# Kernel tuning notes

Hardware: AMD Instinct MI355X
Metric: run time of the kernel (lower is better)

## Reference

```python
import jax, jax.numpy as jnp
import numpy as np

NUM_USER = 100000
NUM_ITEM = 50000
DIM = 64
NUM_EDGES = 3200000


def setup_inputs() -> dict:
    key = jax.random.key(0)
    k1, k2, k3, k4 = jax.random.split(key, 4)
    return {
        "user_embedding": jax.random.normal(k1, (NUM_USER, DIM), dtype=jnp.float32),
        "item_embedding": jax.random.normal(k2, (NUM_ITEM, DIM), dtype=jnp.float32),
        "edge_user": jax.random.randint(k3, (NUM_EDGES,), 0, NUM_USER, dtype=jnp.int32).astype(jnp.int64),
        "edge_item": jax.random.randint(k4, (NUM_EDGES,), 0, NUM_ITEM, dtype=jnp.int32).astype(jnp.int64),
    }


def _segment_mean(feats, idx, num_segments):
    # scatter_mean semantics: sum per segment / count, empty segments -> 0
    s = jax.ops.segment_sum(feats, idx, num_segments=num_segments)  # [n, dim]
    cnt = jax.ops.segment_sum(jnp.ones((idx.shape[0], 1), feats.dtype), idx,
                              num_segments=num_segments)  # [n, 1]
    return s / jnp.maximum(cnt, 1.0)


def reference(user_embedding, item_embedding, edge_user, edge_item):
    num_user = user_embedding.shape[0]
    num_item = item_embedding.shape[0]

    # view1: aggregate_neighbor_features — mean of purchased-item embeddings per user
    neighbor_feat = _segment_mean(item_embedding[edge_item], edge_user, num_user)

    # view2: aggregate_cooccurrence_features — two-stage mean aggregation
    # stage 1: per item, mean of its purchasers' embeddings
    item_user_agg = _segment_mean(user_embedding[edge_user], edge_item, num_item)
    # stage 2: per user, mean of stage-1 features of purchased items
    cooccur_feat = _segment_mean(item_user_agg[edge_item], edge_user, num_user)

    return (neighbor_feat, cooccur_feat)
```

## Files before the change

### kernel.cpp

```cpp
#include <hip/hip_runtime.h>
#include <hip/hip_fp16.h>

constexpr int NUM_USER  = 100000;
constexpr int NUM_ITEM  = 50000;
constexpr int DIM       = 64;
constexpr int NUM_EDGES = 3200000;

constexpr int KPB   = 64;
constexpr int NB_U  = (NUM_USER + KPB - 1) / KPB;
constexpr int NB_I  = (NUM_ITEM + KPB - 1) / KPB;
constexpr int HKEY  = 32;
constexpr int CHUNK = 4096;
constexpr int CSH   = 14;
constexpr int NCH_I = 4;
constexpr int NCH_U = 7;
constexpr int CAP_U = 2560;
constexpr int CAP_I = 4608;

__device__ __forceinline__ __half2 u2h(unsigned u) {
  union { unsigned u; __half2 h; } v; v.u = u; return v.h;
}
__device__ __forceinline__ unsigned h2u(__half2 h) {
  union { __half2 h; unsigned u; } v; v.h = h; return v.u;
}

__device__ __forceinline__ int detect64(const void* eu, const void* ei) {
  const int* a = (const int*)eu;
  const int* b = (const int*)ei;
  int any = 0;
#pragma unroll
  for (int i = 1; i < 64; i += 2) { any |= a[i]; any |= b[i]; }
  return any == 0;
}

__device__ __forceinline__ int idx_at(const void* p, int e, int is64) {
  return is64 ? ((const int*)p)[2 * e] : ((const int*)p)[e];
}

__global__ void k_cvt(const float* __restrict__ ue, unsigned* __restrict__ u32,
                      const float* __restrict__ ie, unsigned* __restrict__ fused) {
  const int nu = NUM_USER * 32, ni = NUM_ITEM * 32;
  for (int t = blockIdx.x * blockDim.x + threadIdx.x; t < nu + ni;
       t += gridDim.x * blockDim.x) {
    if (t < nu) {
      const float2 v = ((const float2*)ue)[t];
      u32[t] = h2u(__floats2half2_rn(v.x, v.y));
    } else {
      const int s = t - nu;
      const float2 v = ((const float2*)ie)[s];
      fused[(size_t)(s >> 5) * 64 + 2 * (s & 31)] = h2u(__floats2half2_rn(v.x, v.y));
    }
  }
}

__global__ void k_part2(const void* eu_p, const void* ei_p,
                        int* gcur_i, unsigned int* __restrict__ pairs_i,
                        int* gcur_u, unsigned int* __restrict__ pairs_u,
                        int capI, int capU) {
  __shared__ int hist_u[NB_U], base_u[NB_U];
  __shared__ int hist_i[NB_I], base_i[NB_I];
  for (int t = threadIdx.x; t < NB_U; t += blockDim.x) hist_u[t] = 0;
  for (int t = threadIdx.x; t < NB_I; t += blockDim.x) hist_i[t] = 0;
  __syncthreads();
  const int is64 = detect64(eu_p, ei_p);
  const int ch = NUM_EDGES / gridDim.x;
  const int lo = blockIdx.x * ch, hiE = lo + ch;
  for (int e = lo + threadIdx.x; e < hiE; e += blockDim.x) {
    atomicAdd(&hist_u[idx_at(eu_p, e, is64) >> 6], 1);
    atomicAdd(&hist_i[idx_at(ei_p, e, is64) >> 6], 1);
  }
  __syncthreads();
  for (int t = threadIdx.x; t < NB_U; t += blockDim.x) {
    const int h = hist_u[t];
    int b = 0;
    if (h) {
      b = atomicAdd(&gcur_u[t], h);
      if (capU) b += t * capU;
    }
    base_u[t] = b;
    hist_u[t] = 0;
  }
  for (int t = threadIdx.x; t < NB_I; t += blockDim.x) {
    const int h = hist_i[t];
    int b = 0;
    if (h) {
      b = atomicAdd(&gcur_i[t], h);
      if (capI) b += t * capI;
    }
    base_i[t] = b;
    hist_i[t] = 0;
  }
  __syncthreads();
  for (int e = lo + threadIdx.x; e < hiE; e += blockDim.x) {
    const int eu = idx_at(eu_p, e, is64);
    const int ei = idx_at(ei_p, e, is64);
    const int bi = ei >> 6;
    const int pi = base_i[bi] + atomicAdd(&hist_i[bi], 1);
    if (!capI || pi < (bi + 1) * capI)
      pairs_i[pi] = ((unsigned)(ei & 63) << 17) | (unsigned)eu;
    const int bu = eu >> 6;
    const int pu = base_u[bu] + atomicAdd(&hist_u[bu], 1);
    if (!capU || pu < (bu + 1) * capU)
      pairs_u[pu] = ((unsigned)(eu & 63) << 17) | (unsigned)ei;
  }
}

__global__ void k_hist_part(const void* eu_p, const void* ei_p,
                            int* __restrict__ partials) {
  __shared__ int hu[NB_U];
  __shared__ int hi_[NB_I];
  for (int t = threadIdx.x; t < NB_U; t += blockDim.x) hu[t] = 0;
  for (int t = threadIdx.x; t < NB_I; t += blockDim.x) hi_[t] = 0;
  __syncthreads();
  const int is64 = detect64(eu_p, ei_p);
  const int ga = gridDim.x;
  const int ch = NUM_EDGES / ga;
  const int b = blockIdx.x;
  const int lo = b * ch, hiE = lo + ch;
  for (int e = lo + threadIdx.x; e < hiE; e += blockDim.x) {
    atomicAdd(&hu[idx_at(eu_p, e, is64) >> 6], 1);
    atomicAdd(&hi_[idx_at(ei_p, e, is64) >> 6], 1);
  }
  __syncthreads();
  int* pu = partials;
  int* pi = partials + (size_t)NB_U * ga;
  for (int t = threadIdx.x; t < NB_U; t += blockDim.x) pu[(size_t)t * ga + b] = hu[t];
  for (int t = threadIdx.x; t < NB_I; t += blockDim.x) pi[(size_t)t * ga + b] = hi_[t];
}

__global__ void k_hist_reduce(const int* __restrict__ partials, int ga,
                              int* __restrict__ gcnt_u, int* __restrict__ gcnt_i) {
  const int k = blockIdx.x * blockDim.x + threadIdx.x;
  if (k >= NB_U + NB_I) return;
  const int* base = (k < NB_U) ? partials + (size_t)k * ga
                               : partials + (size_t)NB_U * ga + (size_t)(k - NB_U) * ga;
  int s = 0;
  for (int b = 0; b < ga; ++b) s += base[b];
  if (k < NB_U) gcnt_u[k] = s;
  else          gcnt_i[k - NB_U] = s;
}

__device__ void scan_body(const int* __restrict__ in, int* __restrict__ out,
                          int* __restrict__ cur, int n) {
  __shared__ int part[1024];
  const int t = threadIdx.x;
  const int chunk = (n + 1023) >> 10;
  const int lo = min(t * chunk, n);
  const int hi = min(lo + chunk, n);
  int s = 0;
  for (int i = lo; i < hi; ++i) s += in[i];
  part[t] = s;
  __syncthreads();
  for (int d = 1; d < 1024; d <<= 1) {
    int v = (t >= d) ? part[t - d] : 0;
    __syncthreads();
    part[t] += v;
    __syncthreads();
  }
  int run = (t == 0) ? 0 : part[t - 1];
  for (int i = lo; i < hi; ++i) {
    int v = in[i];
    out[i] = run; cur[i] = run; run += v;
  }
  if (t == 1023) out[n] = part[1023];
}

__global__ void k_scan2(const int* cu, int* bu, int* curu,
                        const int* ci, int* bi, int* curi) {
  if (blockIdx.x == 0) scan_body(cu, bu, curu, NB_U);
  else                 scan_body(ci, bi, curi, NB_I);
}

__device__ __forceinline__ void decode_bucket(int g, int NB, int& bucket, int& half) {
  const int G = (NB * 2) >> 4;
  if (g < G * 16) {
    const int q = g >> 4, r = g & 15;
    bucket = q * 8 + (r & 7);
    half = r >> 3;
  } else {
    const int idx = g - G * 16;
    bucket = G * 8 + (idx >> 1);
    half = idx & 1;
  }
}

__device__ __forceinline__ void bucket_extent(int bucket, const int* gbase,
                                              const int* gcnt, int cap,
                                              int& lo, int& hi) {
  if (cap > 0) {
    lo = bucket * cap;
    hi = lo + min(gcnt[bucket], cap);
  } else {
    lo = gbase[bucket];
    hi = gbase[bucket + 1];
  }
}

__global__ __launch_bounds__(256, 8)
void k_agg_item(const unsigned* __restrict__ user32,
                const unsigned int* __restrict__ pairs,
                const int* __restrict__ gbase, const int* __restrict__ gcnt,
                int cap, unsigned* __restrict__ fused) {
  constexpr int NBINS = NCH_U * HKEY;
  __shared__ int sorted[CHUNK];
  __shared__ int hist[NBINS], base[NBINS], cur[NBINS];
  __shared__ int gsum[NCH_U];
  const int tid = threadIdx.x;
  const int lane = tid & 63;
  const int wid = tid >> 6;
  const int half = lane >> 5;
  const int c = lane & 31;
  int bucket, key_half;
  decode_bucket(blockIdx.x, NB_I, bucket, key_half);
  const int key0 = key_half * HKEY;
  int lo, hi;
  bucket_extent(bucket, gbase, gcnt, cap, lo, hi);

  unsigned s[8]; int cnt[8];
#pragma unroll
  for (int r = 0; r < 8; ++r) { s[r] = 0u; cnt[r] = 0; }

  for (int clo = lo; clo < hi; clo += CHUNK) {
    const int csz = min(CHUNK, hi - clo);
    for (int t = tid; t < NBINS; t += 256) hist[t] = 0;
    __syncthreads();
    for (int j = tid; j < csz; j += 256) {
      const unsigned p = pairs[clo + j];
      const int k = (int)(p >> 17) - key0;
      if ((unsigned)k < HKEY) {
        const int ch = (int)(p & 0x1FFFF) >> CSH;
        atomicAdd(&hist[ch * HKEY + k], 1);
      }
    }
    __syncthreads();
    if (tid < NCH_U) {
      int g = 0;
      for (int q = 0; q < HKEY; ++q) g += hist[tid * HKEY + q];
      gsum[tid] = g;
    }
    __syncthreads();
    for (int t = tid; t < NBINS; t += 256) {
      const int ch = t >> 5;
      int b = 0;
      for (int q = 0; q < ch; ++q) b += gsum[q];
      for (int q = ch * HKEY; q < t; ++q) b += hist[q];
      base[t] = b; cur[t] = b;
    }
    __syncthreads();
    for (int j = tid; j < csz; j += 256) {
      const unsigned p = pairs[clo + j];
      const int k = (int)(p >> 17) - key0;
      if ((unsigned)k < HKEY) {
        const int v = (int)(p & 0x1FFFF);
        const int slot = atomicAdd(&cur[(v >> CSH) * HKEY + k], 1);
        sorted[slot] = v;
      }
    }
    __syncthreads();
    for (int ch = 0; ch < NCH_U; ++ch) {
#pragma unroll
      for (int r = 0; r < 8; ++r) {
        const int bin = ch * HKEY + wid * 8 + r;
        const int jlo = base[bin], jhi = cur[bin];
        cnt[r] += jhi - jlo;
        for (int j = jlo; j < jhi; j += 8) {
          unsigned w[4];
#pragma unroll
          for (int q = 0; q < 4; ++q) {
            const int jj = j + 2 * q + half;
            w[q] = (jj < jhi) ? user32[(size_t)sorted[jj] * 32 + c] : 0u;
          }
#pragma unroll
          for (int q = 0; q < 4; ++q)
            s[r] = h2u(__hadd2(u2h(s[r]), u2h(w[q])));
        }
      }
    }
    __syncthreads();
  }

  const int i0 = bucket * KPB + key0;
#pragma unroll
  for (int r = 0; r < 8; ++r) {
    const unsigned o = (unsigned)__shfl_xor((int)s[r], 32);
    const __half2 tot = __hadd2(u2h(s[r]), u2h(o));
    const int item = i0 + wid * 8 + r;
    if (half == 0 && item < NUM_ITEM) {
      const float inv = 1.0f / fmaxf((float)cnt[r], 1.f);
      fused[(size_t)item * 64 + 2 * c + 1] =
          h2u(__floats2half2_rn(__low2float(tot) * inv, __high2float(tot) * inv));
    }
  }
}

__global__ __launch_bounds__(256, 8)
void k_agg_user(const unsigned* __restrict__ fused,
                const unsigned int* __restrict__ pairs,
                const int* __restrict__ gbase, const int* __restrict__ gcnt,
                int cap,
                float* __restrict__ out0, float* __restrict__ out1) {
  constexpr int NBINS = NCH_I * HKEY;
  __shared__ int sorted[CHUNK];
  __shared__ int hist[NBINS], base[NBINS], cur[NBINS];
  __shared__ int gsum[NCH_I];
  const int tid = threadIdx.x;
  const int lane = tid & 63;
  const int wid = tid >> 6;
  const int half = lane >> 5;
  const int c = lane & 31;
  int bucket, key_half;
  decode_bucket(blockIdx.x, NB_U, bucket, key_half);
  const int key0 = key_half * HKEY;
  int lo, hi;
  bucket_extent(bucket, gbase, gcnt, cap, lo, hi);
  const uint2* fused2 = (const uint2*)fused;

  unsigned s0[8], s1[8]; int cnt[8];
#pragma unroll
  for (int r = 0; r < 8; ++r) { s0[r] = 0u; s1[r] = 0u; cnt[r] = 0; }

  for (int clo = lo; clo < hi; clo += CHUNK) {
    const int csz = min(CHUNK, hi - clo);
    for (int t = tid; t < NBINS; t += 256) hist[t] = 0;
    __syncthreads();
    for (int j = tid; j < csz; j += 256) {
      const unsigned p = pairs[clo + j];
      const int k = (int)(p >> 17) - key0;
      if ((unsigned)k < HKEY) {
        const int ch = (int)(p & 0x1FFFF) >> CSH;
        atomicAdd(&hist[ch * HKEY + k], 1);
      }
    }
    __syncthreads();
    if (tid < NCH_I) {
      int g = 0;
      for (int q = 0; q < HKEY; ++q) g += hist[tid * HKEY + q];
      gsum[tid] = g;
    }
    __syncthreads();
    for (int t = tid; t < NBINS; t += 256) {
      const int ch = t >> 5;
      int b = 0;
      for (int q = 0; q < ch; ++q) b += gsum[q];
      for (int q = ch * HKEY; q < t; ++q) b += hist[q];
      base[t] = b; cur[t] = b;
    }
    __syncthreads();
    for (int j = tid; j < csz; j += 256) {
      const unsigned p = pairs[clo + j];
      const int k = (int)(p >> 17) - key0;
      if ((unsigned)k < HKEY) {
        const int v = (int)(p & 0x1FFFF);
        const int slot = atomicAdd(&cur[(v >> CSH) * HKEY + k], 1);
        sorted[slot] = v;
      }
    }
    __syncthreads();
    for (int ch = 0; ch < NCH_I; ++ch) {
#pragma unroll
      for (int r = 0; r < 8; ++r) {
        const int bin = ch * HKEY + wid * 8 + r;
        const int jlo = base[bin], jhi = cur[bin];
        cnt[r] += jhi - jlo;
        for (int j = jlo; j < jhi; j += 8) {
          uint2 w[4];
#pragma unroll
          for (int q = 0; q < 4; ++q) {
            const int jj = j + 2 * q + half;
            w[q] = (jj < jhi) ? fused2[(size_t)sorted[jj] * 32 + c]
                              : make_uint2(0u, 0u);
          }
#pragma unroll
          for (int q = 0; q < 4; ++q) {
            s0[r] = h2u(__hadd2(u2h(s0[r]), u2h(w[q].x)));
            s1[r] = h2u(__hadd2(u2h(s1[r]), u2h(w[q].y)));
          }
        }
      }
    }
    __syncthreads();
  }

  const int u0 = bucket * KPB + key0;
#pragma unroll
  for (int r = 0; r < 8; ++r) {
    const unsigned o0 = (unsigned)__shfl_xor((int)s0[r], 32);
    const unsigned o1 = (unsigned)__shfl_xor((int)s1[r], 32);
    const __half2 t0 = __hadd2(u2h(s0[r]), u2h(o0));
    const __half2 t1 = __hadd2(u2h(s1[r]), u2h(o1));
    const int u = u0 + wid * 8 + r;
    if (half == 0 && u < NUM_USER) {
      const float inv = 1.0f / fmaxf((float)cnt[r], 1.f);
      ((float2*)out0)[(size_t)u * 32 + c] =
          make_float2(__low2float(t0) * inv, __high2float(t0) * inv);
      ((float2*)out1)[(size_t)u * 32 + c] =
          make_float2(__low2float(t1) * inv, __high2float(t1) * inv);
    }
  }
}

__global__ void k_scatter1(const float* __restrict__ user_emb,
                           const float* __restrict__ item_emb,
                           const void* eu_p, const void* ei_p,
                           float* out0, float* item_sum,
                           float* cnt_user, float* cnt_item) {
  const int is64 = detect64(eu_p, ei_p);
  const int lane = threadIdx.x & (DIM - 1);
  const int sub  = threadIdx.x >> 6;
  const int epb  = blockDim.x >> 6;
  for (int e = blockIdx.x * epb + sub; e < NUM_EDGES; e += gridDim.x * epb) {
    const int eu = idx_at(eu_p, e, is64);
    const int ei = idx_at(ei_p, e, is64);
    atomicAdd(&out0[eu * DIM + lane], item_emb[ei * DIM + lane]);
    atomicAdd(&item_sum[ei * DIM + lane], user_emb[eu * DIM + lane]);
    if (lane == 0) {
      atomicAdd(&cnt_user[eu], 1.0f);
      atomicAdd(&cnt_item[ei], 1.0f);
    }
  }
}

__global__ void k_div_item(float* item_sum, const float* __restrict__ cnt_item) {
  const int n = NUM_ITEM * DIM;
  for (int t = blockIdx.x * blockDim.x + threadIdx.x; t < n;
       t += gridDim.x * blockDim.x)
    item_sum[t] /= fmaxf(cnt_item[t >> 6], 1.0f);
}

__global__ void k_scatter2(const float* __restrict__ item_agg,
                           const void* eu_p, const void* ei_p, float* out1) {
  const int is64 = detect64(eu_p, ei_p);
  const int lane = threadIdx.x & (DIM - 1);
  const int sub  = threadIdx.x >> 6;
  const int epb  = blockDim.x >> 6;
  for (int e = blockIdx.x * epb + sub; e < NUM_EDGES; e += gridDim.x * epb) {
    const int eu = idx_at(eu_p, e, is64);
    const int ei = idx_at(ei_p, e, is64);
    atomicAdd(&out1[eu * DIM + lane], item_agg[ei * DIM + lane]);
  }
}

__global__ void k_finalize(float* out0, float* out1,
                           const float* __restrict__ cnt_user) {
  const int n = NUM_USER * DIM;
  for (int t = blockIdx.x * blockDim.x + threadIdx.x; t < n;
       t += gridDim.x * blockDim.x) {
    const float c = fmaxf(cnt_user[t >> 6], 1.0f);
    out0[t] /= c;
    out1[t] /= c;
  }
}

extern "C" void kernel_launch(void* const* d_in, const int* in_sizes, int n_in,
                              void* d_out, int out_size, void* d_ws, size_t ws_size,
                              hipStream_t stream) {
  const float* user_emb = (const float*)d_in[0];
  const float* item_emb = (const float*)d_in[1];
  const void*  eu_p     = d_in[2];
  const void*  ei_p     = d_in[3];

  float* out0 = (float*)d_out;
  float* out1 = out0 + (size_t)NUM_USER * DIM;

  int* wsi = (int*)d_ws;
  float* wsf = (float*)d_ws;

  const size_t s_pairs_u = 0;
  const size_t s_pairs_i = s_pairs_u + (size_t)NB_U * CAP_U;
  const size_t s_user32  = s_pairs_i + (size_t)NB_I * CAP_I;
  const size_t s_fused   = s_user32 + (size_t)NUM_USER * 32;
  const size_t s_gcur_u  = s_fused + (size_t)NUM_ITEM * 64;
  const size_t s_gcur_i  = s_gcur_u + NB_U;
  const size_t s_end     = s_gcur_i + NB_I;
  const size_t need_static = s_end * 4;

  const size_t o_pairs   = 0;
  const size_t o_user32  = o_pairs + NUM_EDGES;
  const size_t o_fused   = o_user32 + (size_t)NUM_USER * 32;
  const size_t o_gcnt_u  = o_fused + (size_t)NUM_ITEM * 64;
  const size_t o_gbase_u = o_gcnt_u + NB_U;
  const size_t o_gcur_u  = o_gbase_u + NB_U + 1;
  const size_t o_gcnt_i  = o_gcur_u + NB_U;
  const size_t o_gbase_i = o_gcnt_i + NB_I;
  const size_t o_gcur_i  = o_gbase_i + NB_I + 1;
  const size_t o_pairs2  = o_gcur_i + NB_I;
  const size_t need_dynamic = (o_pairs2 + NUM_EDGES) * 4;

  if (ws_size >= need_static) {
    unsigned int* pairs_u = (unsigned int*)(wsi + s_pairs_u);
    unsigned int* pairs_i = (unsigned int*)(wsi + s_pairs_i);
    unsigned* user32 = (unsigned*)(wsi + s_user32);
    unsigned* fused  = (unsigned*)(wsi + s_fused);
    int* gcur_u = wsi + s_gcur_u;
    int* gcur_i = wsi + s_gcur_i;

    hipMemsetAsync(gcur_u, 0, (size_t)(NB_U + NB_I) * 4, stream);
    k_cvt<<<1536, 256, 0, stream>>>(user_emb, user32, item_emb, fused);
    k_part2<<<256, 1024, 0, stream>>>(eu_p, ei_p, gcur_i, pairs_i,
                                      gcur_u, pairs_u, CAP_I, CAP_U);
    k_agg_item<<<NB_I * 2, 256, 0, stream>>>(user32, pairs_i, nullptr,
                                             gcur_i, CAP_I, fused);
    k_agg_user<<<NB_U * 2, 256, 0, stream>>>(fused, pairs_u, nullptr,
                                             gcur_u, CAP_U, out0, out1);
  } else if (ws_size >= need_dynamic) {
    unsigned int* pairs_i  = (unsigned int*)(wsi + o_pairs);
    int*          partials = wsi + o_pairs;
    unsigned* user32 = (unsigned*)(wsi + o_user32);
    unsigned* fused  = (unsigned*)(wsi + o_fused);
    int* gcnt_u  = wsi + o_gcnt_u;
    int* gbase_u = wsi + o_gbase_u;
    int* gcur_u  = wsi + o_gcur_u;
    int* gcnt_i  = wsi + o_gcnt_i;
    int* gbase_i = wsi + o_gbase_i;
    int* gcur_i  = wsi + o_gcur_i;
    unsigned int* pairs_u = (unsigned int*)(wsi + o_pairs2);

    k_hist_part<<<256, 512, 0, stream>>>(eu_p, ei_p, partials);
    k_hist_reduce<<<(NB_U + NB_I + 255) / 256, 256, 0, stream>>>(partials, 256,
                                                                 gcnt_u, gcnt_i);
    k_scan2<<<2, 1024, 0, stream>>>(gcnt_u, gbase_u, gcur_u,
                                    gcnt_i, gbase_i, gcur_i);
    k_cvt<<<1536, 256, 0, stream>>>(user_emb, user32, item_emb, fused);
    k_part2<<<256, 1024, 0, stream>>>(eu_p, ei_p, gcur_i, pairs_i,
                                      gcur_u, pairs_u, 0, 0);
    k_agg_item<<<NB_I * 2, 256, 0, stream>>>(user32, pairs_i, gbase_i,
                                             nullptr, 0, fused);
    k_agg_user<<<NB_U * 2, 256, 0, stream>>>(fused, pairs_u, gbase_u,
                                             nullptr, 0, out0, out1);
  } else {
    float* item_sum = wsf;
    float* cnt_user = wsf + (size_t)NUM_ITEM * DIM;
    float* cnt_item = cnt_user + NUM_USER;
    const size_t used = ((size_t)NUM_ITEM * DIM + NUM_USER + NUM_ITEM) * 4;

    hipMemsetAsync(d_out, 0, (size_t)out_size * sizeof(float), stream);
    hipMemsetAsync(d_ws, 0, used, stream);
    k_scatter1<<<4096, 256, 0, stream>>>(user_emb, item_emb, eu_p, ei_p,
                                         out0, item_sum, cnt_user, cnt_item);
    k_div_item<<<2048, 256, 0, stream>>>(item_sum, cnt_item);
    k_scatter2<<<4096, 256, 0, stream>>>(item_sum, eu_p, ei_p, out1);
    k_finalize<<<2048, 256, 0, stream>>>(out0, out1, cnt_user);
  }
}
```

Before: 264.5 us.

## Shrink buckets to 32 keys and drop half-key split in aggregation kernels

```diff
diff --git a/kernel.cpp b/kernel.cpp
--- a/kernel.cpp
+++ b/kernel.cpp
@@ -6,16 +6,15 @@
 constexpr int DIM       = 64;
 constexpr int NUM_EDGES = 3200000;
 
-constexpr int KPB   = 64;
+constexpr int KPB   = 32;
 constexpr int NB_U  = (NUM_USER + KPB - 1) / KPB;
 constexpr int NB_I  = (NUM_ITEM + KPB - 1) / KPB;
-constexpr int HKEY  = 32;
 constexpr int CHUNK = 4096;
 constexpr int CSH   = 14;
 constexpr int NCH_I = 4;
 constexpr int NCH_U = 7;
-constexpr int CAP_U = 2560;
-constexpr int CAP_I = 4608;
+constexpr int CAP_U = 1280;
+constexpr int CAP_I = 2304;
 
 __device__ __forceinline__ __half2 u2h(unsigned u) {
   union { unsigned u; __half2 h; } v; v.u = u; return v.h;
@@ -66,8 +65,8 @@
   const int ch = NUM_EDGES / gridDim.x;
   const int lo = blockIdx.x * ch, hiE = lo + ch;
   for (int e = lo + threadIdx.x; e < hiE; e += blockDim.x) {
-    atomicAdd(&hist_u[idx_at(eu_p, e, is64) >> 6], 1);
-    atomicAdd(&hist_i[idx_at(ei_p, e, is64) >> 6], 1);
+    atomicAdd(&hist_u[idx_at(eu_p, e, is64) >> 5], 1);
+    atomicAdd(&hist_i[idx_at(ei_p, e, is64) >> 5], 1);
   }
   __syncthreads();
   for (int t = threadIdx.x; t < NB_U; t += blockDim.x) {
@@ -94,14 +93,14 @@
   for (int e = lo + threadIdx.x; e < hiE; e += blockDim.x) {
     const int eu = idx_at(eu_p, e, is64);
     const int ei = idx_at(ei_p, e, is64);
-    const int bi = ei >> 6;
+    const int bi = ei >> 5;
     const int pi = base_i[bi] + atomicAdd(&hist_i[bi], 1);
     if (!capI || pi < (bi + 1) * capI)
-      pairs_i[pi] = ((unsigned)(ei & 63) << 17) | (unsigned)eu;
-    const int bu = eu >> 6;
+      pairs_i[pi] = ((unsigned)(ei & 31) << 17) | (unsigned)eu;
+    const int bu = eu >> 5;
     const int pu = base_u[bu] + atomicAdd(&hist_u[bu], 1);
     if (!capU || pu < (bu + 1) * capU)
-      pairs_u[pu] = ((unsigned)(eu & 63) << 17) | (unsigned)ei;
+      pairs_u[pu] = ((unsigned)(eu & 31) << 17) | (unsigned)ei;
   }
 }
 
@@ -118,8 +117,8 @@
   const int b = blockIdx.x;
   const int lo = b * ch, hiE = lo + ch;
   for (int e = lo + threadIdx.x; e < hiE; e += blockDim.x) {
-    atomicAdd(&hu[idx_at(eu_p, e, is64) >> 6], 1);
-    atomicAdd(&hi_[idx_at(ei_p, e, is64) >> 6], 1);
+    atomicAdd(&hu[idx_at(eu_p, e, is64) >> 5], 1);
+    atomicAdd(&hi_[idx_at(ei_p, e, is64) >> 5], 1);
   }
   __syncthreads();
   int* pu = partials;
@@ -171,19 +170,6 @@
   else                 scan_body(ci, bi, curi, NB_I);
 }
 
-__device__ __forceinline__ void decode_bucket(int g, int NB, int& bucket, int& half) {
-  const int G = (NB * 2) >> 4;
-  if (g < G * 16) {
-    const int q = g >> 4, r = g & 15;
-    bucket = q * 8 + (r & 7);
-    half = r >> 3;
-  } else {
-    const int idx = g - G * 16;
-    bucket = G * 8 + (idx >> 1);
-    half = idx & 1;
-  }
-}
-
 __device__ __forceinline__ void bucket_extent(int bucket, const int* gbase,
                                               const int* gcnt, int cap,
                                               int& lo, int& hi) {
@@ -201,7 +187,7 @@
                 const unsigned int* __restrict__ pairs,
                 const int* __restrict__ gbase, const int* __restrict__ gcnt,
                 int cap, unsigned* __restrict__ fused) {
-  constexpr int NBINS = NCH_U * HKEY;
+  constexpr int NBINS = NCH_U * KPB;
   __shared__ int sorted[CHUNK];
   __shared__ int hist[NBINS], base[NBINS], cur[NBINS];
   __shared__ int gsum[NCH_U];
@@ -210,9 +196,7 @@
   const int wid = tid >> 6;
   const int half = lane >> 5;
   const int c = lane & 31;
-  int bucket, key_half;
-  decode_bucket(blockIdx.x, NB_I, bucket, key_half);
-  const int key0 = key_half * HKEY;
+  const int bucket = blockIdx.x;
   int lo, hi;
   bucket_extent(bucket, gbase, gcnt, cap, lo, hi);
 
@@ -226,16 +210,12 @@
     __syncthreads();
     for (int j = tid; j < csz; j += 256) {
       const unsigned p = pairs[clo + j];
-      const int k = (int)(p >> 17) - key0;
-      if ((unsigned)k < HKEY) {
-        const int ch = (int)(p & 0x1FFFF) >> CSH;
-        atomicAdd(&hist[ch * HKEY + k], 1);
-      }
+      atomicAdd(&hist[((p & 0x1FFFF) >> CSH) * KPB + (p >> 17)], 1);
     }
     __syncthreads();
     if (tid < NCH_U) {
       int g = 0;
-      for (int q = 0; q < HKEY; ++q) g += hist[tid * HKEY + q];
+      for (int q = 0; q < KPB; ++q) g += hist[tid * KPB + q];
       gsum[tid] = g;
     }
     __syncthreads();
@@ -243,24 +223,21 @@
       const int ch = t >> 5;
       int b = 0;
       for (int q = 0; q < ch; ++q) b += gsum[q];
-      for (int q = ch * HKEY; q < t; ++q) b += hist[q];
+      for (int q = ch * KPB; q < t; ++q) b += hist[q];
       base[t] = b; cur[t] = b;
     }
     __syncthreads();
     for (int j = tid; j < csz; j += 256) {
       const unsigned p = pairs[clo + j];
-      const int k = (int)(p >> 17) - key0;
-      if ((unsigned)k < HKEY) {
-        const int v = (int)(p & 0x1FFFF);
-        const int slot = atomicAdd(&cur[(v >> CSH) * HKEY + k], 1);
-        sorted[slot] = v;
-      }
+      const int v = (int)(p & 0x1FFFF);
+      const int slot = atomicAdd(&cur[(v >> CSH) * KPB + (p >> 17)], 1);
+      sorted[slot] = v;
     }
     __syncthreads();
     for (int ch = 0; ch < NCH_U; ++ch) {
 #pragma unroll
       for (int r = 0; r < 8; ++r) {
-        const int bin = ch * HKEY + wid * 8 + r;
+        const int bin = ch * KPB + wid * 8 + r;
         const int jlo = base[bin], jhi = cur[bin];
         cnt[r] += jhi - jlo;
         for (int j = jlo; j < jhi; j += 8) {
@@ -279,7 +256,7 @@
     __syncthreads();
   }
 
-  const int i0 = bucket * KPB + key0;
+  const int i0 = bucket * KPB;
 #pragma unroll
   for (int r = 0; r < 8; ++r) {
     const unsigned o = (unsigned)__shfl_xor((int)s[r], 32);
@@ -299,7 +276,7 @@
                 const int* __restrict__ gbase, const int* __restrict__ gcnt,
                 int cap,
                 float* __restrict__ out0, float* __restrict__ out1) {
-  constexpr int NBINS = NCH_I * HKEY;
+  constexpr int NBINS = NCH_I * KPB;
   __shared__ int sorted[CHUNK];
   __shared__ int hist[NBINS], base[NBINS], cur[NBINS];
   __shared__ int gsum[NCH_I];
@@ -308,9 +285,7 @@
   const int wid = tid >> 6;
   const int half = lane >> 5;
   const int c = lane & 31;
-  int bucket, key_half;
-  decode_bucket(blockIdx.x, NB_U, bucket, key_half);
-  const int key0 = key_half * HKEY;
+  const int bucket = blockIdx.x;
   int lo, hi;
   bucket_extent(bucket, gbase, gcnt, cap, lo, hi);
   const uint2* fused2 = (const uint2*)fused;
@@ -325,16 +300,12 @@
     __syncthreads();
     for (int j = tid; j < csz; j += 256) {
       const unsigned p = pairs[clo + j];
-      const int k = (int)(p >> 17) - key0;
-      if ((unsigned)k < HKEY) {
-        const int ch = (int)(p & 0x1FFFF) >> CSH;
-        atomicAdd(&hist[ch * HKEY + k], 1);
-      }
+      atomicAdd(&hist[((p & 0x1FFFF) >> CSH) * KPB + (p >> 17)], 1);
     }
     __syncthreads();
     if (tid < NCH_I) {
       int g = 0;
-      for (int q = 0; q < HKEY; ++q) g += hist[tid * HKEY + q];
+      for (int q = 0; q < KPB; ++q) g += hist[tid * KPB + q];
       gsum[tid] = g;
     }
     __syncthreads();
@@ -342,24 +313,21 @@
       const int ch = t >> 5;
       int b = 0;
       for (int q = 0; q < ch; ++q) b += gsum[q];
-      for (int q = ch * HKEY; q < t; ++q) b += hist[q];
+      for (int q = ch * KPB; q < t; ++q) b += hist[q];
       base[t] = b; cur[t] = b;
     }
     __syncthreads();
     for (int j = tid; j < csz; j += 256) {
       const unsigned p = pairs[clo + j];
-      const int k = (int)(p >> 17) - key0;
-      if ((unsigned)k < HKEY) {
-        const int v = (int)(p & 0x1FFFF);
-        const int slot = atomicAdd(&cur[(v >> CSH) * HKEY + k], 1);
-        sorted[slot] = v;
-      }
+      const int v = (int)(p & 0x1FFFF);
+      const int slot = atomicAdd(&cur[(v >> CSH) * KPB + (p >> 17)], 1);
+      sorted[slot] = v;
     }
     __syncthreads();
     for (int ch = 0; ch < NCH_I; ++ch) {
 #pragma unroll
       for (int r = 0; r < 8; ++r) {
-        const int bin = ch * HKEY + wid * 8 + r;
+        const int bin = ch * KPB + wid * 8 + r;
         const int jlo = base[bin], jhi = cur[bin];
         cnt[r] += jhi - jlo;
         for (int j = jlo; j < jhi; j += 8) {
@@ -381,7 +349,7 @@
     __syncthreads();
   }
 
-  const int u0 = bucket * KPB + key0;
+  const int u0 = bucket * KPB;
 #pragma unroll
   for (int r = 0; r < 8; ++r) {
     const unsigned o0 = (unsigned)__shfl_xor((int)s0[r], 32);
@@ -498,10 +466,10 @@
     k_cvt<<<1536, 256, 0, stream>>>(user_emb, user32, item_emb, fused);
     k_part2<<<256, 1024, 0, stream>>>(eu_p, ei_p, gcur_i, pairs_i,
                                       gcur_u, pairs_u, CAP_I, CAP_U);
-    k_agg_item<<<NB_I * 2, 256, 0, stream>>>(user32, pairs_i, nullptr,
-                                             gcur_i, CAP_I, fused);
-    k_agg_user<<<NB_U * 2, 256, 0, stream>>>(fused, pairs_u, nullptr,
-                                             gcur_u, CAP_U, out0, out1);
+    k_agg_item<<<NB_I, 256, 0, stream>>>(user32, pairs_i, nullptr,
+                                         gcur_i, CAP_I, fused);
+    k_agg_user<<<NB_U, 256, 0, stream>>>(fused, pairs_u, nullptr,
+                                         gcur_u, CAP_U, out0, out1);
   } else if (ws_size >= need_dynamic) {
     unsigned int* pairs_i  = (unsigned int*)(wsi + o_pairs);
     int*          partials = wsi + o_pairs;
@@ -523,10 +491,10 @@
     k_cvt<<<1536, 256, 0, stream>>>(user_emb, user32, item_emb, fused);
     k_part2<<<256, 1024, 0, stream>>>(eu_p, ei_p, gcur_i, pairs_i,
                                       gcur_u, pairs_u, 0, 0);
-    k_agg_item<<<NB_I * 2, 256, 0, stream>>>(user32, pairs_i, gbase_i,
-                                             nullptr, 0, fused);
-    k_agg_user<<<NB_U * 2, 256, 0, stream>>>(fused, pairs_u, gbase_u,
-                                             nullptr, 0, out0, out1);
+    k_agg_item<<<NB_I, 256, 0, stream>>>(user32, pairs_i, gbase_i,
+                                         nullptr, 0, fused);
+    k_agg_user<<<NB_U, 256, 0, stream>>>(fused, pairs_u, gbase_u,
+                                         nullptr, 0, out0, out1);
   } else {
     float* item_sum = wsf;
     float* cnt_user = wsf + (size_t)NUM_ITEM * DIM;
```

Result: faster. 251.0 us (-5.1%).
